# Performance work log

Hardware: AMD Instinct MI355X
Metric: run time of the kernel (lower is better)

The kernel has to match this reference:

```python
import jax, jax.numpy as jnp
import numpy as np

B, C, H, W = 8, 64, 256, 256
KERNEL_SIZE = 19
DILATION = 1
RADIUS = (KERNEL_SIZE - 1) // 2  # 9
BN_EPS = 1e-5


def setup_inputs() -> dict:
    key = jax.random.key(0)
    k1, k2 = jax.random.split(key, 2)
    x = jax.random.normal(k1, (B, C, H, W), dtype=jnp.float32)
    dw_kernel = jax.random.normal(k2, (C, 1, 3, 3), dtype=jnp.float32) * 0.1
    gamma = jnp.ones((C,), dtype=jnp.float32)
    beta = jnp.zeros((C,), dtype=jnp.float32)
    return {"x": x, "dw_kernel": dw_kernel, "gamma": gamma, "beta": beta}


def _diag_strip_sum(x):
    # zero-padded diagonal shift-and-sum over offsets -R..R (step=dilation)
    r = RADIUS
    h, w = x.shape[2], x.shape[3]
    xp = jnp.pad(x, ((0, 0), (0, 0), (r, r), (r, r)))
    acc = jnp.zeros_like(x)
    for i in range(-r, r + 1, DILATION):
        acc = acc + xp[:, :, r + i:r + i + h, r + i:r + i + w]
    n_taps = 2 * r // DILATION + 1
    return acc / n_taps


def reference(x, dw_kernel, gamma, beta):
    xs = _diag_strip_sum(x)  # [B,C,H,W]
    # depthwise 3x3 conv, padding=1, no bias
    y = jax.lax.conv_general_dilated(
        xs, dw_kernel, window_strides=(1, 1), padding=((1, 1), (1, 1)),
        dimension_numbers=("NCHW", "OIHW", "NCHW"),
        feature_group_count=xs.shape[1])
    # BatchNorm2d (training mode: batch stats, biased variance)
    mean = y.mean(axis=(0, 2, 3), keepdims=True)
    var = y.var(axis=(0, 2, 3), keepdims=True)
    yn = (y - mean) * jax.lax.rsqrt(var + BN_EPS)
    yn = yn * gamma[None, :, None, None] + beta[None, :, None, None]
    return jax.nn.gelu(yn, approximate=False)
```

## Files before the change

### kernel.cpp

```cpp
#include <hip/hip_runtime.h>
#include <math.h>

#define BB 8
#define CC 64
#define HH 256
#define WW 256
constexpr int TILE_H = 32;
constexpr int TILE_W = 64;
constexpr int RAD    = 9;
constexpr int HALO   = RAD + 1;
constexpr int NR     = TILE_H + 2 * HALO;
constexpr int NC     = 88;
constexpr int COL0   = 12;
constexpr int SNR    = TILE_H + 2;
constexpr int SNC    = TILE_W + 2;
constexpr int SS     = 68;
constexpr float INV_TAPS = 1.0f / 19.0f;
constexpr float BN_EPS = 1e-5f;

__device__ double g_stats[2 * CC];

template <int PASS>
__global__ __launch_bounds__(256) void fused_kernel(
    const float* __restrict__ x,
    const float* __restrict__ wk,
    const float* __restrict__ gamma,
    const float* __restrict__ beta,
    float* __restrict__ out)
{
    __shared__ float IN[NR][NC];
    __shared__ float S[SNR][SS];
    __shared__ float red[8];

    const int bid  = blockIdx.x;
    const int tcol = bid & 3;
    const int trow = (bid >> 2) & 7;
    const int ch   = (bid >> 5) & 63;
    const int b    = bid >> 11;
    const int th   = trow * TILE_H;
    const int tw   = tcol * TILE_W;
    const int tid  = threadIdx.x;

    const float* __restrict__ xp = x + (size_t)(b * CC + ch) * (HH * WW);

    float wgt[9];
#pragma unroll
    for (int k = 0; k < 9; ++k) wgt[k] = wk[ch * 9 + k] * INV_TAPS;

    for (int idx = tid; idx < NR * (NC / 4); idx += 256) {
        int r  = idx / (NC / 4);
        int c4 = idx - r * (NC / 4);
        int gh = th - HALO + r;
        int gw = tw - COL0 + (c4 << 2);
        float4 v = make_float4(0.f, 0.f, 0.f, 0.f);
        if ((unsigned)gh < HH && (unsigned)gw < WW)
            v = *(const float4*)&xp[gh * WW + gw];
        *(float4*)&IN[r][c4 << 2] = v;
    }
    __syncthreads();

    for (int seg = tid; seg < 9 * 69; seg += 256) {
        int bi  = seg / 69;
        int sj0 = (seg - bi * 69) - 3;
        int si0 = bi * 4;
        int t0  = sj0 < 0 ? -sj0 : 0;
        int tmax = SNR - si0; if (tmax > 4) tmax = 4;
        if (SNC - sj0 < tmax) tmax = SNC - sj0;
        if (t0 < tmax) {
            int si = si0 + t0, sj = sj0 + t0;
            int gr = th + si - 1, gc = tw + sj - 1;
            float run = 0.f;
#pragma unroll
            for (int k = 0; k < 19; ++k) run += IN[si + k][sj + 2 + k];
            S[si][sj] = ((unsigned)gr < HH && (unsigned)gc < WW) ? run : 0.f;
            for (int t = t0 + 1; t < tmax; ++t) {
                ++si; ++sj; ++gr; ++gc;
                run += IN[si + 18][sj + 2 + 18] - IN[si - 1][sj + 2 - 1];
                S[si][sj] = ((unsigned)gr < HH && (unsigned)gc < WW) ? run : 0.f;
            }
        }
    }
    __syncthreads();

    const int i0 = tid >> 4;
    const int j4 = (tid & 15) << 2;

    float s1 = 0.f, s2 = 0.f;
    float scale = 0.f, shift = 0.f;
    if (PASS == 1) {
        const double N = (double)BB * HH * WW;
        double mean = g_stats[ch] / N;
        double var  = g_stats[CC + ch] / N - mean * mean;
        scale = gamma[ch] * (float)(1.0 / sqrt(var + (double)BN_EPS));
        shift = beta[ch] - (float)mean * scale;
    }

#pragma unroll
    for (int half = 0; half < 2; ++half) {
        const int i = i0 + half * 16;
        float4 a0 = *(const float4*)&S[i][j4];
        float2 b0 = *(const float2*)&S[i][j4 + 4];
        float4 a1 = *(const float4*)&S[i + 1][j4];
        float2 b1 = *(const float2*)&S[i + 1][j4 + 4];
        float4 a2 = *(const float4*)&S[i + 2][j4];
        float2 b2 = *(const float2*)&S[i + 2][j4 + 4];
        float r0[6] = {a0.x, a0.y, a0.z, a0.w, b0.x, b0.y};
        float r1[6] = {a1.x, a1.y, a1.z, a1.w, b1.x, b1.y};
        float r2[6] = {a2.x, a2.y, a2.z, a2.w, b2.x, b2.y};
        float y[4];
#pragma unroll
        for (int q = 0; q < 4; ++q) {
            y[q] = wgt[0] * r0[q] + wgt[1] * r0[q + 1] + wgt[2] * r0[q + 2]
                 + wgt[3] * r1[q] + wgt[4] * r1[q + 1] + wgt[5] * r1[q + 2]
                 + wgt[6] * r2[q] + wgt[7] * r2[q + 1] + wgt[8] * r2[q + 2];
        }
        if (PASS == 0) {
#pragma unroll
            for (int q = 0; q < 4; ++q) { s1 += y[q]; s2 += y[q] * y[q]; }
        } else {
            float4 o;
#pragma unroll
            for (int q = 0; q < 4; ++q) {
                float v = y[q] * scale + shift;
                ((float*)&o)[q] = 0.5f * v * (1.0f + erff(v * 0.70710678118654752f));
            }
            float* __restrict__ po =
                out + ((size_t)(b * CC + ch) * HH + (th + i)) * WW + tw + j4;
            *(float4*)po = o;
        }
    }

    if (PASS == 0) {
#pragma unroll
        for (int off = 32; off > 0; off >>= 1) {
            s1 += __shfl_down(s1, off);
            s2 += __shfl_down(s2, off);
        }
        if ((tid & 63) == 0) { red[(tid >> 6) * 2] = s1; red[(tid >> 6) * 2 + 1] = s2; }
        __syncthreads();
        if (tid == 0) {
            float t1 = red[0] + red[2] + red[4] + red[6];
            float t2 = red[1] + red[3] + red[5] + red[7];
            atomicAdd(&g_stats[ch], (double)t1);
            atomicAdd(&g_stats[CC + ch], (double)t2);
        }
    }
}

__global__ void zero_stats_kernel() {
    int t = threadIdx.x;
    if (t < 2 * CC) g_stats[t] = 0.0;
}

extern "C" void kernel_launch(void* const* d_in, const int* in_sizes, int n_in,
                              void* d_out, int out_size, void* d_ws, size_t ws_size,
                              hipStream_t stream) {
    const float* x     = (const float*)d_in[0];
    const float* wk    = (const float*)d_in[1];
    const float* gamma = (const float*)d_in[2];
    const float* beta  = (const float*)d_in[3];
    float* out = (float*)d_out;

    const int nblocks = BB * CC * (HH / TILE_H) * (WW / TILE_W);

    zero_stats_kernel<<<1, 128, 0, stream>>>();
    fused_kernel<0><<<nblocks, 256, 0, stream>>>(x, wk, gamma, beta, nullptr);
    fused_kernel<1><<<nblocks, 256, 0, stream>>>(x, wk, gamma, beta, out);
}
```

Measured before the change: 353.4 us.

## Materialize conv output in workspace and apply BN+GELU in streaming pass

Pass 0 now writes the pre-normalization conv output y to the workspace buffer, and a new elementwise kernel reads y to apply batch-norm and GELU. This replaces the second full recomputation of the diagonal strip sum and 3x3 conv, including the haloed tile loads. In exchange it costs an extra 128MB write and read of y. The old two-pass recompute path stays as a fallback when the workspace is too small.

```diff
diff --git a/kernel.cpp b/kernel.cpp
--- a/kernel.cpp
+++ b/kernel.cpp
@@ -17,10 +17,11 @@
 constexpr int SS     = 68;
 constexpr float INV_TAPS = 1.0f / 19.0f;
 constexpr float BN_EPS = 1e-5f;
+constexpr size_t Y_BYTES = (size_t)BB * CC * HH * WW * sizeof(float);
 
 __device__ double g_stats[2 * CC];
 
-template <int PASS>
+template <int PASS, bool STORE_Y>
 __global__ __launch_bounds__(256) void fused_kernel(
     const float* __restrict__ x,
     const float* __restrict__ wk,
@@ -117,6 +118,11 @@
         if (PASS == 0) {
 #pragma unroll
             for (int q = 0; q < 4; ++q) { s1 += y[q]; s2 += y[q] * y[q]; }
+            if (STORE_Y) {
+                float* __restrict__ po =
+                    out + ((size_t)(b * CC + ch) * HH + (th + i)) * WW + tw + j4;
+                *(float4*)po = make_float4(y[0], y[1], y[2], y[3]);
+            }
         } else {
             float4 o;
 #pragma unroll
@@ -144,6 +150,40 @@
             atomicAdd(&g_stats[ch], (double)t1);
             atomicAdd(&g_stats[CC + ch], (double)t2);
         }
+    }
+}
+
+__global__ __launch_bounds__(256) void bn_gelu_kernel(
+    const float* __restrict__ y,
+    const float* __restrict__ gamma,
+    const float* __restrict__ beta,
+    float* __restrict__ out)
+{
+    const int plane = blockIdx.x >> 2;
+    const int part  = blockIdx.x & 3;
+    const int ch    = plane & 63;
+
+    const double N = (double)BB * HH * WW;
+    double mean = g_stats[ch] / N;
+    double var  = g_stats[CC + ch] / N - mean * mean;
+    const float scale = gamma[ch] * (float)(1.0 / sqrt(var + (double)BN_EPS));
+    const float shift = beta[ch] - (float)mean * scale;
+
+    const size_t base = (size_t)plane * (HH * WW) + (size_t)part * (HH * WW / 4);
+    const float4* __restrict__ yp = (const float4*)(y + base);
+    float4* __restrict__ op = (float4*)(out + base);
+
+#pragma unroll
+    for (int it = 0; it < 16; ++it) {
+        int i = threadIdx.x + it * 256;
+        float4 v = yp[i];
+        float4 o;
+#pragma unroll
+        for (int q = 0; q < 4; ++q) {
+            float t = ((const float*)&v)[q] * scale + shift;
+            ((float*)&o)[q] = 0.5f * t * (1.0f + erff(t * 0.70710678118654752f));
+        }
+        op[i] = o;
     }
 }
 
@@ -164,6 +204,12 @@
     const int nblocks = BB * CC * (HH / TILE_H) * (WW / TILE_W);
 
     zero_stats_kernel<<<1, 128, 0, stream>>>();
-    fused_kernel<0><<<nblocks, 256, 0, stream>>>(x, wk, gamma, beta, nullptr);
-    fused_kernel<1><<<nblocks, 256, 0, stream>>>(x, wk, gamma, beta, out);
-}
+    if (ws_size >= Y_BYTES) {
+        float* yw = (float*)d_ws;
+        fused_kernel<0, true><<<nblocks, 256, 0, stream>>>(x, wk, gamma, beta, yw);
+        bn_gelu_kernel<<<BB * CC * 4, 256, 0, stream>>>(yw, gamma, beta, out);
+    } else {
+        fused_kernel<0, false><<<nblocks, 256, 0, stream>>>(x, wk, gamma, beta, nullptr);
+        fused_kernel<1, false><<<nblocks, 256, 0, stream>>>(x, wk, gamma, beta, out);
+    }
+}
```

Result: faster. 328.3 us (-7.1%).
